# Kernel tuning notes

Hardware: AMD Instinct MI355X
Metric: run time of the kernel (lower is better)

Reference implementation:

```python
import jax, jax.numpy as jnp
import numpy as np

N_DIM = 768
HIDDEN_DIM = 768
BATCH = 4
SEQ = 2048


def setup_inputs() -> dict:
    key = jax.random.key(0)
    ks = jax.random.split(key, 9)
    s_in = 1.0 / np.sqrt(N_DIM)
    s_h = 1.0 / np.sqrt(HIDDEN_DIM)
    return {
        "x": jax.random.normal(ks[0], (BATCH, SEQ, N_DIM), dtype=jnp.float32),
        # torch Linear weights: [out_features, in_features]
        "wq": jax.random.uniform(ks[1], (HIDDEN_DIM, N_DIM), jnp.float32, -s_in, s_in),
        "bq": jax.random.uniform(ks[2], (HIDDEN_DIM,), jnp.float32, -s_in, s_in),
        "wk": jax.random.uniform(ks[3], (HIDDEN_DIM, N_DIM), jnp.float32, -s_in, s_in),
        "bk": jax.random.uniform(ks[4], (HIDDEN_DIM,), jnp.float32, -s_in, s_in),
        "wv": jax.random.uniform(ks[5], (HIDDEN_DIM, N_DIM), jnp.float32, -s_in, s_in),
        "bv": jax.random.uniform(ks[6], (HIDDEN_DIM,), jnp.float32, -s_in, s_in),
        "wo": jax.random.uniform(ks[7], (N_DIM, HIDDEN_DIM), jnp.float32, -s_h, s_h),
        "bo": jax.random.uniform(ks[8], (N_DIM,), jnp.float32, -s_h, s_h),
    }


def reference(x, wq, bq, wk, bk, wv, bv, wo, bo):
    # q,k,v: [B, S, H]
    q = jnp.einsum("bsd,hd->bsh", x, wq) + bq
    k = jnp.einsum("bsd,hd->bsh", x, wk) + bk
    v = jnp.einsum("bsd,hd->bsh", x, wv) + bv
    # NOTE: faithful to source — no 1/sqrt(d) scaling, no mask.
    scores = jnp.einsum("bqh,bkh->bqk", q, k)  # [B, S, S]
    attn = jax.nn.softmax(scores, axis=-1)
    y = jnp.einsum("bqk,bkh->bqh", attn, v)  # [B, S, H]
    out = jnp.einsum("bsh,dh->bsd", y, wo) + bo
    return out
```

## Files before the change

### kernel.cpp

```cpp
#include <hip/hip_runtime.h>

typedef _Float16 f16;
typedef _Float16 f16x8 __attribute__((ext_vector_type(8)));
typedef float f32x4 __attribute__((ext_vector_type(4)));

#define GLD16(g, l) __builtin_amdgcn_global_load_lds( \
    (const __attribute__((address_space(1))) void*)(g), \
    (__attribute__((address_space(3))) void*)(l), 16, 0, 0)

template <typename OutT, int BM, int BN, int MODE, int MINW>
__global__ __launch_bounds__(256, MINW)
void gemm_kernel(const f16* __restrict__ A, long sA,
                 const f16* __restrict__ B, long sB,
                 void* __restrict__ Cv, long sC,
                 void* __restrict__ C2v,
                 const float* __restrict__ bias,
                 const float* __restrict__ bias2,
                 int N, int K)
{
    constexpr int FM = BM / 32;
    constexpr int FN = BN / 32;
    constexpr int IA = BM / 32;
    constexpr int IB = BN / 32;

    OutT* C  = (OutT*)Cv;
    OutT* C2 = (OutT*)C2v;
    const int tid  = threadIdx.x;
    const int wave = tid >> 6;
    const int lane = tid & 63;
    const int bz   = blockIdx.z;
    A += (long)bz * sA;
    B += (long)bz * sB;
    C += (long)bz * sC;
    const long bm = (long)blockIdx.x * BM;
    const long bn = (long)blockIdx.y * BN;

    __shared__ f16 sAt[BM * 64];
    __shared__ f16 sBt[BN * 64];

    const int srow = lane >> 3;
    const int gch  = ((lane & 7) ^ srow) * 8;

    const f16* gAb = A + (bm + wave * (BM / 4) + srow) * (long)K + gch;
    const f16* gBb = B + (bn + wave * (BN / 4) + srow) * (long)K + gch;

    const int wm = (wave >> 1) * (BM / 2);
    const int wn = (wave & 1) * (BN / 2);
    const int lr = lane & 15;
    const int qd = lane >> 4;
    const int swz0 = ((0 * 4 + qd) ^ (lr & 7)) * 8;
    const int swz1 = ((1 * 4 + qd) ^ (lr & 7)) * 8;

    f32x4 acc[FM][FN] = {};

    for (int k0 = 0; k0 < K; k0 += 64) {
        #pragma unroll
        for (int i = 0; i < IA; ++i)
            GLD16(gAb + k0 + (long)i * 8 * K, &sAt[(wave * (BM / 4) + i * 8) * 64]);
        #pragma unroll
        for (int i = 0; i < IB; ++i)
            GLD16(gBb + k0 + (long)i * 8 * K, &sBt[(wave * (BN / 4) + i * 8) * 64]);
        __syncthreads();

        #pragma unroll
        for (int h = 0; h < 2; ++h) {
            const int swz = h ? swz1 : swz0;
            f16x8 af[FM], bf[FN];
            #pragma unroll
            for (int t = 0; t < FM; ++t)
                af[t] = *(const f16x8*)&sAt[(wm + t * 16 + lr) * 64 + swz];
            #pragma unroll
            for (int t = 0; t < FN; ++t)
                bf[t] = *(const f16x8*)&sBt[(wn + t * 16 + lr) * 64 + swz];
            #pragma unroll
            for (int tm = 0; tm < FM; ++tm)
                #pragma unroll
                for (int tn = 0; tn < FN; ++tn)
                    acc[tm][tn] = __builtin_amdgcn_mfma_f32_16x16x32_f16(
                        af[tm], bf[tn], acc[tm][tn], 0, 0, 0);
        }
        __syncthreads();
    }

    #pragma unroll
    for (int tn = 0; tn < FN; ++tn) {
        const long col = bn + wn + tn * 16 + lr;
        OutT* dst = C;
        long cc = col, stride = N;
        float bc = 0.f;
        if (MODE == 1) bc = bias[col];
        if (MODE == 3) {
            stride = 768;
            if (col >= 768) { dst = C2; cc = col - 768; bc = bias2[cc]; }
            else            { bc = bias[cc]; }
        }
        #pragma unroll
        for (int tm = 0; tm < FM; ++tm) {
            #pragma unroll
            for (int r = 0; r < 4; ++r) {
                const long row = bm + wm + tm * 16 + qd * 4 + r;
                float v = acc[tm][tn][r] + bc;
                if (MODE == 2) v += bias[row];
                dst[row * stride + cc] = (OutT)v;
            }
        }
    }
}

__global__ __launch_bounds__(256)
void softmax_kernel(f16* __restrict__ S)
{
    const long row = blockIdx.x;
    f16* p = S + row * 2048;
    const int tid  = threadIdx.x;
    const int wave = tid >> 6;
    const int lane = tid & 63;

    f16x8 x = *(const f16x8*)&p[tid * 8];
    float v[8];
    float m = -1e30f;
    #pragma unroll
    for (int j = 0; j < 8; ++j) { v[j] = (float)x[j]; m = fmaxf(m, v[j]); }
    #pragma unroll
    for (int off = 32; off > 0; off >>= 1) m = fmaxf(m, __shfl_down(m, off));

    __shared__ float rm[4], rs[4];
    if (lane == 0) rm[wave] = m;
    __syncthreads();
    m = fmaxf(fmaxf(rm[0], rm[1]), fmaxf(rm[2], rm[3]));

    float s = 0.f;
    #pragma unroll
    for (int j = 0; j < 8; ++j) { v[j] = __expf(v[j] - m); s += v[j]; }
    #pragma unroll
    for (int off = 32; off > 0; off >>= 1) s += __shfl_down(s, off);
    if (lane == 0) rs[wave] = s;
    __syncthreads();
    s = rs[0] + rs[1] + rs[2] + rs[3];
    const float inv = 1.0f / s;

    f16x8 y;
    #pragma unroll
    for (int j = 0; j < 8; ++j) y[j] = (f16)(v[j] * inv);
    *(f16x8*)&p[tid * 8] = y;
}

__global__ __launch_bounds__(256)
void cvt_all_kernel(const float* __restrict__ x,
                    const float* __restrict__ w0, const float* __restrict__ w1,
                    const float* __restrict__ w2, const float* __restrict__ w3,
                    f16* __restrict__ x16, f16* __restrict__ w16)
{
    const float* in; f16* out; long i;
    if (blockIdx.x < 3072) {
        in = x; out = x16;
        i = ((long)blockIdx.x * 256 + threadIdx.x) * 8;
    } else {
        const int wb  = blockIdx.x - 3072;
        const int sel = wb / 288;
        in  = (sel == 0) ? w0 : (sel == 1) ? w1 : (sel == 2) ? w2 : w3;
        out = w16 + (long)sel * 589824;
        i = ((long)(wb - sel * 288) * 256 + threadIdx.x) * 8;
    }
    float4 a = *(const float4*)(in + i);
    float4 b = *(const float4*)(in + i + 4);
    f16x8 o;
    o[0] = (f16)a.x; o[1] = (f16)a.y; o[2] = (f16)a.z; o[3] = (f16)a.w;
    o[4] = (f16)b.x; o[5] = (f16)b.y; o[6] = (f16)b.z; o[7] = (f16)b.w;
    *(f16x8*)&out[i] = o;
}

extern "C" void kernel_launch(void* const* d_in, const int* in_sizes, int n_in,
                              void* d_out, int out_size, void* d_ws, size_t ws_size,
                              hipStream_t stream)
{
    const float* x  = (const float*)d_in[0];
    const float* wq = (const float*)d_in[1];
    const float* bq = (const float*)d_in[2];
    const float* wk = (const float*)d_in[3];
    const float* bk = (const float*)d_in[4];
    const float* wv = (const float*)d_in[5];
    const float* bv = (const float*)d_in[6];
    const float* wo = (const float*)d_in[7];
    const float* bo = (const float*)d_in[8];

    char* ws = (char*)d_ws;
    f16* x16 = (f16*)(ws + 0);
    f16* w16 = (f16*)(ws + 12582912);
    f16* Q   = (f16*)(ws + 17301504);
    f16* Kb  = (f16*)(ws + 29884416);
    f16* VT  = (f16*)(ws + 42467328);
    f16* S   = (f16*)(ws + 55050240);
    f16* Y   = (f16*)(ws + 88604672);

    f16* wv16 = w16 + 2 * 589824;
    f16* wo16 = w16 + 3 * 589824;

    cvt_all_kernel<<<4224, 256, 0, stream>>>(x, wq, wk, wv, wo, x16, w16);

    gemm_kernel<f16, 128, 128, 3, 3><<<dim3(64, 12, 1), 256, 0, stream>>>(
        x16, 0, w16, 0, Q, 0, Kb, bq, bk, 1536, 768);
    gemm_kernel<f16, 64, 128, 2, 4><<<dim3(12, 16, 4), 256, 0, stream>>>(
        wv16, 0, x16, (long)2048 * 768, VT, (long)768 * 2048, nullptr,
        bv, nullptr, 2048, 768);
    gemm_kernel<f16, 128, 256, 0, 2><<<dim3(16, 8, 4), 256, 0, stream>>>(
        Q, (long)2048 * 768, Kb, (long)2048 * 768, S, (long)2048 * 2048,
        nullptr, nullptr, nullptr, 2048, 768);
    softmax_kernel<<<8192, 256, 0, stream>>>(S);
    gemm_kernel<f16, 128, 64, 0, 4><<<dim3(16, 12, 4), 256, 0, stream>>>(
        S, (long)2048 * 2048, VT, (long)768 * 2048, Y, (long)2048 * 768,
        nullptr, nullptr, nullptr, 768, 2048);
    gemm_kernel<float, 128, 64, 1, 4><<<dim3(64, 12, 1), 256, 0, stream>>>(
        Y, 0, wo16, 0, (float*)d_out, 0, nullptr, bo, nullptr, 768, 768);
}
```

Measured before the change: 230.0 us.

## Add double-buffered 256x256 GEMM for QK^T and enlarge tiles of other GEMMs

Introduces a 512-thread GEMM kernel with 256x256 tiles and double-buffered LDS, so the global-to-LDS loads for the next K slice are issued while MFMAs run on the current one. It also raises wave priority around the MFMA block. It is used for the Q·K^T score GEMM. The V projection, attn·V and output GEMMs move to 128x128 tiles, which reduces grid size and improves operand reuse. The trade-off is 128KB of LDS per block, which may limit occupancy, and fewer blocks for the smaller GEMMs.

New measurement: 244.5 us. 6.3% more time.

```diff
diff --git a/kernel.cpp b/kernel.cpp
--- a/kernel.cpp
+++ b/kernel.cpp
@@ -107,6 +107,99 @@
     }
 }
 
+__global__ __launch_bounds__(512, 2)
+void gemm_pipe(const f16* __restrict__ A, long sA,
+               const f16* __restrict__ B, long sB,
+               f16* __restrict__ C, long sC,
+               int N, int K)
+{
+    const int tid  = threadIdx.x;
+    const int wave = tid >> 6;
+    const int lane = tid & 63;
+    const int bz   = blockIdx.z;
+    A += (long)bz * sA;
+    B += (long)bz * sB;
+    C += (long)bz * sC;
+    const long bm = (long)blockIdx.x * 256;
+    const long bn = (long)blockIdx.y * 256;
+
+    __shared__ f16 sAt[2][256 * 64];
+    __shared__ f16 sBt[2][256 * 64];
+
+    const int srow = lane >> 3;
+    const int gch  = ((lane & 7) ^ srow) * 8;
+    const f16* gA = A + (bm + wave * 32 + srow) * (long)K + gch;
+    const f16* gB = B + (bn + wave * 32 + srow) * (long)K + gch;
+
+    const int wm = (wave >> 2) * 128;
+    const int wn = (wave & 3) * 64;
+    const int lr = lane & 15;
+    const int qd = lane >> 4;
+    const int swz0 = ((0 * 4 + qd) ^ (lr & 7)) * 8;
+    const int swz1 = ((1 * 4 + qd) ^ (lr & 7)) * 8;
+
+    f32x4 acc[8][4] = {};
+
+    #pragma unroll
+    for (int i = 0; i < 4; ++i)
+        GLD16(gA + (long)i * 8 * K, &sAt[0][(wave * 32 + i * 8) * 64]);
+    #pragma unroll
+    for (int i = 0; i < 4; ++i)
+        GLD16(gB + (long)i * 8 * K, &sBt[0][(wave * 32 + i * 8) * 64]);
+    __syncthreads();
+
+    const int nt = K / 64;
+    for (int t = 0; t < nt; ++t) {
+        const int cur = t & 1;
+        if (t + 1 < nt) {
+            const long off = (long)(t + 1) * 64;
+            #pragma unroll
+            for (int i = 0; i < 4; ++i)
+                GLD16(gA + off + (long)i * 8 * K, &sAt[cur ^ 1][(wave * 32 + i * 8) * 64]);
+            #pragma unroll
+            for (int i = 0; i < 4; ++i)
+                GLD16(gB + off + (long)i * 8 * K, &sBt[cur ^ 1][(wave * 32 + i * 8) * 64]);
+        }
+        #pragma unroll
+        for (int h = 0; h < 2; ++h) {
+            const int swz = h ? swz1 : swz0;
+            f16x8 bf[4];
+            #pragma unroll
+            for (int c = 0; c < 4; ++c)
+                bf[c] = *(const f16x8*)&sBt[cur][(wn + c * 16 + lr) * 64 + swz];
+            #pragma unroll
+            for (int rh = 0; rh < 2; ++rh) {
+                f16x8 af[4];
+                #pragma unroll
+                for (int m = 0; m < 4; ++m)
+                    af[m] = *(const f16x8*)&sAt[cur][(wm + rh * 64 + m * 16 + lr) * 64 + swz];
+                __builtin_amdgcn_s_setprio(1);
+                #pragma unroll
+                for (int m = 0; m < 4; ++m)
+                    #pragma unroll
+                    for (int c = 0; c < 4; ++c)
+                        acc[rh * 4 + m][c] = __builtin_amdgcn_mfma_f32_16x16x32_f16(
+                            af[m], bf[c], acc[rh * 4 + m][c], 0, 0, 0);
+                __builtin_amdgcn_s_setprio(0);
+            }
+        }
+        __syncthreads();
+    }
+
+    #pragma unroll
+    for (int cf = 0; cf < 4; ++cf) {
+        const long col = bn + wn + cf * 16 + lr;
+        #pragma unroll
+        for (int rf = 0; rf < 8; ++rf) {
+            #pragma unroll
+            for (int r = 0; r < 4; ++r) {
+                const long row = bm + wm + rf * 16 + qd * 4 + r;
+                C[row * (long)N + col] = (f16)acc[rf][cf][r];
+            }
+        }
+    }
+}
+
 __global__ __launch_bounds__(256)
 void softmax_kernel(f16* __restrict__ S)
 {
@@ -200,16 +293,16 @@
 
     gemm_kernel<f16, 128, 128, 3, 3><<<dim3(64, 12, 1), 256, 0, stream>>>(
         x16, 0, w16, 0, Q, 0, Kb, bq, bk, 1536, 768);
-    gemm_kernel<f16, 64, 128, 2, 4><<<dim3(12, 16, 4), 256, 0, stream>>>(
+    gemm_kernel<f16, 128, 128, 2, 3><<<dim3(6, 16, 4), 256, 0, stream>>>(
         wv16, 0, x16, (long)2048 * 768, VT, (long)768 * 2048, nullptr,
         bv, nullptr, 2048, 768);
-    gemm_kernel<f16, 128, 256, 0, 2><<<dim3(16, 8, 4), 256, 0, stream>>>(
+    gemm_pipe<<<dim3(8, 8, 4), 512, 0, stream>>>(
         Q, (long)2048 * 768, Kb, (long)2048 * 768, S, (long)2048 * 2048,
-        nullptr, nullptr, nullptr, 2048, 768);
+        2048, 768);
     softmax_kernel<<<8192, 256, 0, stream>>>(S);
-    gemm_kernel<f16, 128, 64, 0, 4><<<dim3(16, 12, 4), 256, 0, stream>>>(
+    gemm_kernel<f16, 128, 128, 0, 3><<<dim3(16, 6, 4), 256, 0, stream>>>(
         S, (long)2048 * 2048, VT, (long)768 * 2048, Y, (long)2048 * 768,
         nullptr, nullptr, nullptr, 768, 2048);
-    gemm_kernel<float, 128, 64, 1, 4><<<dim3(64, 12, 1), 256, 0, stream>>>(
+    gemm_kernel<float, 128, 128, 1, 3><<<dim3(64, 6, 1), 256, 0, stream>>>(
         Y, 0, wo16, 0, (float*)d_out, 0, nullptr, bo, nullptr, 768, 768);
 }
```

## Fold output projection into value projection by precomputing Wo·Wv

Applied to the files above, without the earlier changes.

Uses associativity to precompute a combined weight Wc = Wo·Wv and bias Wo·bv, so V' = x·Wcᵀ + Wo·bv is computed directly and the attention-times-V GEMM writes the final output with bias bo. This removes the separate output-projection GEMM and the Y intermediate. The cost is a small weight transpose, a 768x768 weight GEMM and a bias matvec per call, plus an extra fp16 rounding of the combined weight that may shift numerics.

Result: slower. 237.8 us (+3.4%).

```diff
diff --git a/kernel.cpp b/kernel.cpp
--- a/kernel.cpp
+++ b/kernel.cpp
@@ -170,6 +170,42 @@
     *(f16x8*)&out[i] = o;
 }
 
+__global__ __launch_bounds__(256)
+void transpose_kernel(const f16* __restrict__ in, f16* __restrict__ out)
+{
+    __shared__ f16 t[64][72];
+    const int r  = threadIdx.x >> 2;
+    const int c0 = (threadIdx.x & 3) * 16;
+    const f16* src = in + ((long)blockIdx.x * 64 + r) * 768 + blockIdx.y * 64 + c0;
+    f16x8 a = *(const f16x8*)src;
+    f16x8 b = *(const f16x8*)(src + 8);
+    #pragma unroll
+    for (int i = 0; i < 8; ++i) { t[r][c0 + i] = a[i]; t[r][c0 + 8 + i] = b[i]; }
+    __syncthreads();
+    f16x8 o1, o2;
+    #pragma unroll
+    for (int i = 0; i < 8; ++i) { o1[i] = t[c0 + i][r]; o2[i] = t[c0 + 8 + i][r]; }
+    f16* dst = out + ((long)blockIdx.y * 64 + r) * 768 + blockIdx.x * 64 + c0;
+    *(f16x8*)dst = o1;
+    *(f16x8*)(dst + 8) = o2;
+}
+
+__global__ __launch_bounds__(256)
+void wobv_kernel(const float* __restrict__ wo, const float* __restrict__ bv,
+                 float* __restrict__ c)
+{
+    const int d = blockIdx.x;
+    const int tid = threadIdx.x;
+    float s = 0.f;
+    for (int h = tid; h < 768; h += 256) s += wo[d * 768 + h] * bv[h];
+    #pragma unroll
+    for (int off = 32; off > 0; off >>= 1) s += __shfl_down(s, off);
+    __shared__ float rs[4];
+    if ((tid & 63) == 0) rs[tid >> 6] = s;
+    __syncthreads();
+    if (tid == 0) c[d] = rs[0] + rs[1] + rs[2] + rs[3];
+}
+
 extern "C" void kernel_launch(void* const* d_in, const int* in_sizes, int n_in,
                               void* d_out, int out_size, void* d_ws, size_t ws_size,
                               hipStream_t stream)
@@ -185,31 +221,36 @@
     const float* bo = (const float*)d_in[8];
 
     char* ws = (char*)d_ws;
-    f16* x16 = (f16*)(ws + 0);
-    f16* w16 = (f16*)(ws + 12582912);
-    f16* Q   = (f16*)(ws + 17301504);
-    f16* Kb  = (f16*)(ws + 29884416);
-    f16* VT  = (f16*)(ws + 42467328);
-    f16* S   = (f16*)(ws + 55050240);
-    f16* Y   = (f16*)(ws + 88604672);
+    f16* x16  = (f16*)(ws + 0);
+    f16* w16  = (f16*)(ws + 12582912);
+    f16* Q    = (f16*)(ws + 17301504);
+    f16* Kb   = (f16*)(ws + 29884416);
+    f16* VWT  = (f16*)(ws + 42467328);
+    f16* S    = (f16*)(ws + 55050240);
+    f16* wvT  = (f16*)(ws + 88604672);
+    f16* Wc   = (f16*)(ws + 89784320);
+    float* cB = (float*)(ws + 90963968);
 
     f16* wv16 = w16 + 2 * 589824;
     f16* wo16 = w16 + 3 * 589824;
 
     cvt_all_kernel<<<4224, 256, 0, stream>>>(x, wq, wk, wv, wo, x16, w16);
+
+    transpose_kernel<<<dim3(12, 12), 256, 0, stream>>>(wv16, wvT);
+    wobv_kernel<<<768, 256, 0, stream>>>(wo, bv, cB);
+    gemm_kernel<f16, 128, 128, 0, 3><<<dim3(6, 6, 1), 256, 0, stream>>>(
+        wo16, 0, wvT, 0, Wc, 0, nullptr, nullptr, nullptr, 768, 768);
 
     gemm_kernel<f16, 128, 128, 3, 3><<<dim3(64, 12, 1), 256, 0, stream>>>(
         x16, 0, w16, 0, Q, 0, Kb, bq, bk, 1536, 768);
     gemm_kernel<f16, 64, 128, 2, 4><<<dim3(12, 16, 4), 256, 0, stream>>>(
-        wv16, 0, x16, (long)2048 * 768, VT, (long)768 * 2048, nullptr,
-        bv, nullptr, 2048, 768);
+        Wc, 0, x16, (long)2048 * 768, VWT, (long)768 * 2048, nullptr,
+        cB, nullptr, 2048, 768);
     gemm_kernel<f16, 128, 256, 0, 2><<<dim3(16, 8, 4), 256, 0, stream>>>(
         Q, (long)2048 * 768, Kb, (long)2048 * 768, S, (long)2048 * 2048,
         nullptr, nullptr, nullptr, 2048, 768);
     softmax_kernel<<<8192, 256, 0, stream>>>(S);
-    gemm_kernel<f16, 128, 64, 0, 4><<<dim3(16, 12, 4), 256, 0, stream>>>(
-        S, (long)2048 * 2048, VT, (long)768 * 2048, Y, (long)2048 * 768,
-        nullptr, nullptr, nullptr, 768, 2048);
-    gemm_kernel<float, 128, 64, 1, 4><<<dim3(64, 12, 1), 256, 0, stream>>>(
-        Y, 0, wo16, 0, (float*)d_out, 0, nullptr, bo, nullptr, 768, 768);
-}
+    gemm_kernel<float, 128, 64, 1, 4><<<dim3(16, 12, 4), 256, 0, stream>>>(
+        S, (long)2048 * 2048, VWT, (long)768 * 2048, d_out, (long)2048 * 768,
+        nullptr, bo, nullptr, 768, 2048);
+}
```
